# Kernel optimization log

Measured on AMD Instinct MI355X. Metric: run time of the kernel, lower is better.

The kernel has to match this reference:

```python
import jax, jax.numpy as jnp
import numpy as np

N = 10000      # nodes
E = 160000     # edges
F_IN = 128     # input_feature
G = 64         # graphs in batch
NC = 10        # num_classes
H1, H2, H3 = 1000, 700, 200


def _xavier(k, fi, fo):
    lim = float(np.sqrt(6.0 / (fi + fo)))
    return jax.random.uniform(k, (fi, fo), jnp.float32, -lim, lim)


def setup_inputs() -> dict:
    key = jax.random.key(0)
    ks = jax.random.split(key, 8)
    x = jax.random.normal(ks[0], (N, F_IN), jnp.float32)
    edge_index = jax.random.randint(ks[1], (2, E), 0, N)
    batch = jnp.sort(jax.random.randint(ks[2], (N,), 0, G))
    return {
        "x": x,
        "edge_index": edge_index,
        "batch": batch,
        "W1": _xavier(ks[3], F_IN, H1), "b1": jnp.zeros((H1,), jnp.float32),
        "W2": _xavier(ks[4], H1, H2),   "b2": jnp.zeros((H2,), jnp.float32),
        "W3": _xavier(ks[5], H2, H3),   "b3": jnp.zeros((H3,), jnp.float32),
        "Wl": _xavier(ks[6], H3, NC),   "bl": jnp.zeros((NC,), jnp.float32),
    }


def _gcn_conv(x, W, b, src, dst, dinv):
    # GCNConv: h = xW; out_i = sum_{j->i} d_j^-1/2 d_i^-1/2 h_j + d_i^-1 h_i + b
    h = x @ W
    coef = dinv[src] * dinv[dst]                      # [E]
    agg = jax.ops.segment_sum(h[src] * coef[:, None], dst, num_segments=N)
    agg = agg + h * (dinv * dinv)[:, None]            # self-loop term
    return agg + b


def reference(x, edge_index, batch, W1, b1, W2, b2, W3, b3, Wl, bl):
    src, dst = edge_index[0], edge_index[1]
    # degree with self-loops (edge weight 1), computed on target nodes
    deg = jax.ops.segment_sum(jnp.ones((E,), x.dtype), dst, num_segments=N) + 1.0
    dinv = jax.lax.rsqrt(deg)

    h = jax.nn.relu(_gcn_conv(x, W1, b1, src, dst, dinv))
    h = jax.nn.relu(_gcn_conv(h, W2, b2, src, dst, dinv))
    h = jax.nn.relu(_gcn_conv(h, W3, b3, src, dst, dinv))

    # global_mean_pool over graph ids
    s = jax.ops.segment_sum(h, batch, num_segments=G)
    cnt = jax.ops.segment_sum(jnp.ones((N,), h.dtype), batch, num_segments=G)
    pooled = s / jnp.maximum(cnt, 1.0)[:, None]

    # dropout is identity in eval mode
    return pooled @ Wl + bl
```

## Files before the change

### kernel.cpp

```cpp
#include <hip/hip_runtime.h>
#include <hip/hip_bf16.h>
#include <stdint.h>


#define SLOT 64

__device__ __forceinline__ uint16_t f2b(float f) {
    union { float f; uint32_t u; } v; v.f = f;
    return (uint16_t)((v.u + 0x7fffu + ((v.u >> 16) & 1u)) >> 16);
}
__device__ __forceinline__ float blo(uint32_t u) { union { uint32_t u; float f; } v; v.u = u << 16; return v.f; }
__device__ __forceinline__ float bhi(uint32_t u) { union { uint32_t u; float f; } v; v.u = u & 0xffff0000u; return v.f; }

__global__ void k_scatter(const int* __restrict__ src, const int* __restrict__ dst,
                          int* __restrict__ cursor, int* __restrict__ slots, int E) {
    int e = blockIdx.x * blockDim.x + threadIdx.x;
    if (e < E) {
        int s = src[e], d = dst[e];
        int pos = atomicAdd(&cursor[d], 1);
        if (pos < SLOT) slots[d * SLOT + pos] = s;
    }
}
__global__ void k_dinv(const int* __restrict__ deg, float* __restrict__ dinv, int N) {
    int i = blockIdx.x * blockDim.x + threadIdx.x;
    if (i < N) dinv[i] = rsqrtf((float)deg[i] + 1.0f);
}

__global__ void k_prep(const float* __restrict__ W1, const float* __restrict__ W2,
                       const float* __restrict__ W3,
                       uint16_t* __restrict__ T1, uint16_t* __restrict__ T2,
                       uint16_t* __restrict__ T3,
                       const float* __restrict__ b1, const float* __restrict__ b2,
                       const float* __restrict__ b3,
                       float* __restrict__ p1, float* __restrict__ p2,
                       float* __restrict__ p3,
                       const float* __restrict__ x, uint16_t* __restrict__ xb,
                       int F, int H1, int H2, int H3,
                       int Fp, int H1p, int H2p, int H3p, int n8) {
    __shared__ float tile[32][33];
    int z = blockIdx.z;
    if (z < 3) {
        const float* W; uint16_t* T; int K, Nn, Kp, Np;
        if (z == 0)      { W = W1; T = T1; K = F;  Nn = H1; Kp = Fp;  Np = H1p; }
        else if (z == 1) { W = W2; T = T2; K = H1; Nn = H2; Kp = H1p; Np = H2p; }
        else             { W = W3; T = T3; K = H2; Nn = H3; Kp = H2p; Np = H3p; }
        if ((int)blockIdx.x * 32 >= Kp || (int)blockIdx.y * 32 >= Np) return;
        int k0 = blockIdx.x * 32, n0 = blockIdx.y * 32;
        int tx = threadIdx.x, ty = threadIdx.y;
        for (int i = ty; i < 32; i += 8) {
            int k = k0 + i, n = n0 + tx;
            tile[i][tx] = (k < K && n < Nn) ? W[(size_t)k * Nn + n] : 0.f;
        }
        __syncthreads();
        for (int i = ty; i < 32; i += 8) {
            int n = n0 + i, k = k0 + tx;
            T[(size_t)n * Kp + k] = f2b(tile[tx][i]);
        }
    } else {
        int id = (blockIdx.y * gridDim.x + blockIdx.x) * 256 + threadIdx.y * 32 + threadIdx.x;
        if (z == 3) {
            if (id < H1p) p1[id] = (id < H1) ? b1[id] : 0.f;
            else if (id < H1p + H2p) { int k = id - H1p; p2[k] = (k < H2) ? b2[k] : 0.f; }
            else if (id < H1p + H2p + H3p) { int k = id - H1p - H2p; p3[k] = (k < H3) ? b3[k] : 0.f; }
        } else {
            if (id < n8) {
                const float4* x4 = (const float4*)x;
                float4 a = x4[2 * id], b = x4[2 * id + 1];
                uint4 o;
                o.x = (uint32_t)f2b(a.x) | ((uint32_t)f2b(a.y) << 16);
                o.y = (uint32_t)f2b(a.z) | ((uint32_t)f2b(a.w) << 16);
                o.z = (uint32_t)f2b(b.x) | ((uint32_t)f2b(b.y) << 16);
                o.w = (uint32_t)f2b(b.z) | ((uint32_t)f2b(b.w) << 16);
                ((uint4*)xb)[id] = o;
            }
        }
    }
}

__global__ __launch_bounds__(256) void k_agg_panel(
    const uint16_t* __restrict__ in, void* __restrict__ out,
    const int* __restrict__ deg_, const int* __restrict__ slots,
    const float* __restrict__ dinv, const float* __restrict__ bias,
    int N, int Hc, int pc, int P, int relu, int out_f32) {
    int slot  = blockIdx.x & 7;
    int panel = slot % P;
    int seg   = slot / P;
    int nseg  = 8 / P;
    int segLen = (N + nseg - 1) / nseg;
    int idx = (blockIdx.x >> 3) * 256 + threadIdx.x;
    int rel = idx / pc;
    if (rel >= segLen) return;
    int node = seg * segLen + rel;
    if (node >= N) return;
    int j = panel * pc + (idx - rel * pc);
    int deg = deg_[node];
    if (deg > SLOT) deg = SLOT;
    int base = node * SLOT;
    float dv = dinv[node];
    float self = dv * dv;
    const uint4* in4 = (const uint4*)in;
    uint4 v = in4[(size_t)node * Hc + j];
    float a[8];
    a[0] = self * blo(v.x); a[1] = self * bhi(v.x);
    a[2] = self * blo(v.y); a[3] = self * bhi(v.y);
    a[4] = self * blo(v.z); a[5] = self * bhi(v.z);
    a[6] = self * blo(v.w); a[7] = self * bhi(v.w);
    int e = 0;
    for (; e + 2 <= deg; e += 2) {
        int s0 = slots[base + e], s1 = slots[base + e + 1];
        uint4 h0 = in4[(size_t)s0 * Hc + j];
        uint4 h1 = in4[(size_t)s1 * Hc + j];
        float c0 = dinv[s0] * dv, c1 = dinv[s1] * dv;
        a[0] += c0 * blo(h0.x); a[1] += c0 * bhi(h0.x);
        a[2] += c0 * blo(h0.y); a[3] += c0 * bhi(h0.y);
        a[4] += c0 * blo(h0.z); a[5] += c0 * bhi(h0.z);
        a[6] += c0 * blo(h0.w); a[7] += c0 * bhi(h0.w);
        a[0] += c1 * blo(h1.x); a[1] += c1 * bhi(h1.x);
        a[2] += c1 * blo(h1.y); a[3] += c1 * bhi(h1.y);
        a[4] += c1 * blo(h1.z); a[5] += c1 * bhi(h1.z);
        a[6] += c1 * blo(h1.w); a[7] += c1 * bhi(h1.w);
    }
    if (e < deg) {
        int s0 = slots[base + e];
        uint4 h = in4[(size_t)s0 * Hc + j];
        float c = dinv[s0] * dv;
        a[0] += c * blo(h.x); a[1] += c * bhi(h.x);
        a[2] += c * blo(h.y); a[3] += c * bhi(h.y);
        a[4] += c * blo(h.z); a[5] += c * bhi(h.z);
        a[6] += c * blo(h.w); a[7] += c * bhi(h.w);
    }
    if (bias) {
        const float4* b4 = (const float4*)bias;
        float4 b0 = b4[2 * j], b1 = b4[2 * j + 1];
        a[0] += b0.x; a[1] += b0.y; a[2] += b0.z; a[3] += b0.w;
        a[4] += b1.x; a[5] += b1.y; a[6] += b1.z; a[7] += b1.w;
    }
    if (relu) {
#pragma unroll
        for (int t = 0; t < 8; ++t) a[t] = fmaxf(a[t], 0.f);
    }
    if (out_f32) {
        float4* o4 = (float4*)out;
        float4 o0; o0.x = a[0]; o0.y = a[1]; o0.z = a[2]; o0.w = a[3];
        float4 o1; o1.x = a[4]; o1.y = a[5]; o1.z = a[6]; o1.w = a[7];
        o4[(size_t)node * (Hc * 2) + 2 * j]     = o0;
        o4[(size_t)node * (Hc * 2) + 2 * j + 1] = o1;
    } else {
        uint4 o;
        o.x = (uint32_t)f2b(a[0]) | ((uint32_t)f2b(a[1]) << 16);
        o.y = (uint32_t)f2b(a[2]) | ((uint32_t)f2b(a[3]) << 16);
        o.z = (uint32_t)f2b(a[4]) | ((uint32_t)f2b(a[5]) << 16);
        o.w = (uint32_t)f2b(a[6]) | ((uint32_t)f2b(a[7]) << 16);
        ((uint4*)out)[(size_t)node * Hc + j] = o;
    }
}

__global__ __launch_bounds__(256) void k_pool_fast(
    const uint16_t* __restrict__ h, const int* __restrict__ batch,
    float* __restrict__ pooled_sum, int N, int H, int Hp) {
    int j    = threadIdx.x & 63;
    int slot = threadIdx.x >> 6;
    int Hc   = H >> 2;
    if (j >= Hc) return;
    int HcP  = Hp >> 2;
    const uint2* h2 = (const uint2*)h;
    int base = (blockIdx.x * 4 + slot) * 16;
    float a0 = 0.f, a1 = 0.f, a2 = 0.f, a3 = 0.f;
    int gcur = -1;
#pragma unroll 4
    for (int t = 0; t < 16; ++t) {
        int node = base + t;
        if (node < N) {
            int g = batch[node];
            if (g != gcur) {
                if (gcur >= 0) {
                    float* ps = &pooled_sum[(size_t)gcur * H + j * 4];
                    atomicAdd(&ps[0], a0); atomicAdd(&ps[1], a1);
                    atomicAdd(&ps[2], a2); atomicAdd(&ps[3], a3);
                }
                gcur = g; a0 = a1 = a2 = a3 = 0.f;
            }
            uint2 v = h2[(size_t)node * HcP + j];
            a0 += blo(v.x); a1 += bhi(v.x);
            a2 += blo(v.y); a3 += bhi(v.y);
        }
    }
    if (gcur >= 0) {
        float* ps = &pooled_sum[(size_t)gcur * H + j * 4];
        atomicAdd(&ps[0], a0); atomicAdd(&ps[1], a1);
        atomicAdd(&ps[2], a2); atomicAdd(&ps[3], a3);
    }
}

typedef __attribute__((ext_vector_type(8))) short short8;
typedef __attribute__((ext_vector_type(4))) float floatx4;

#define LDSP(p) ((__attribute__((address_space(3))) void*)(uintptr_t)(p))
#define GLBP(p) ((const __attribute__((address_space(1))) void*)(uintptr_t)(p))

__global__ __launch_bounds__(256) void k_gemm_bf16(
    const uint16_t* __restrict__ A, const uint16_t* __restrict__ Bt,
    const float* __restrict__ bias, void* __restrict__ Cout,
    int M, int Kp, int Np, int relu, int out_bf16) {
    __shared__ uint16_t As[128 * 64];
    __shared__ uint16_t Bs[128 * 64];
    int tid = threadIdx.x;
    int wave = tid >> 6, lane = tid & 63;
    int quad = lane >> 4, m16 = lane & 15;
    int wr = wave >> 1, wc = wave & 1;
    int row0 = blockIdx.y * 128, col0 = blockIdx.x * 128;

    int rA = tid >> 3;
    int cA = (tid & 7) ^ (rA & 7);
    const uint16_t* gA = A  + (size_t)(row0 + rA) * Kp + cA * 8;
    const uint16_t* gB = Bt + (size_t)(col0 + rA) * Kp + cA * 8;
    uint16_t* lA = As + tid * 8;
    uint16_t* lB = Bs + tid * 8;
    size_t rowStep32 = (size_t)32 * Kp;

    floatx4 acc[4][4];
#pragma unroll
    for (int i = 0; i < 4; ++i)
#pragma unroll
        for (int j = 0; j < 4; ++j) acc[i][j] = (floatx4){0.f, 0.f, 0.f, 0.f};

    const short* Ash = (const short*)As;
    const short* Bsh = (const short*)Bs;
    int swA = m16 & 7;

    for (int k0 = 0; k0 < Kp; k0 += 64) {
#pragma unroll
        for (int p = 0; p < 4; ++p) {
            __builtin_amdgcn_global_load_lds(GLBP(gA + p * rowStep32), LDSP(lA + p * 2048), 16, 0, 0);
            __builtin_amdgcn_global_load_lds(GLBP(gB + p * rowStep32), LDSP(lB + p * 2048), 16, 0, 0);
        }
        gA += 64; gB += 64;
        __syncthreads();
#pragma unroll
        for (int h = 0; h < 2; ++h) {
            short8 af[4], bf[4];
            int c = h * 4 + quad;
            int pos = (c ^ swA) * 8;
#pragma unroll
            for (int i = 0; i < 4; ++i)
                af[i] = *(const short8*)&Ash[(wr * 64 + i * 16 + m16) * 64 + pos];
#pragma unroll
            for (int j = 0; j < 4; ++j)
                bf[j] = *(const short8*)&Bsh[(wc * 64 + j * 16 + m16) * 64 + pos];
#pragma unroll
            for (int i = 0; i < 4; ++i)
#pragma unroll
                for (int j = 0; j < 4; ++j)
                    acc[i][j] = __builtin_amdgcn_mfma_f32_16x16x32_bf16(af[i], bf[j], acc[i][j], 0, 0, 0);
        }
        __syncthreads();
    }

    float bv[4];
#pragma unroll
    for (int j = 0; j < 4; ++j) {
        int n = col0 + wc * 64 + j * 16 + m16;
        bv[j] = bias ? bias[n] : 0.f;
    }
#pragma unroll
    for (int i = 0; i < 4; ++i) {
        int mBase = row0 + wr * 64 + i * 16 + quad * 4;
#pragma unroll
        for (int r = 0; r < 4; ++r) {
            int m = mBase + r;
            if (m < M) {
#pragma unroll
                for (int j = 0; j < 4; ++j) {
                    int n = col0 + wc * 64 + j * 16 + m16;
                    float v = acc[i][j][r] + bv[j];
                    if (relu) v = fmaxf(v, 0.f);
                    if (out_bf16) ((uint16_t*)Cout)[(size_t)m * Np + n] = f2b(v);
                    else          ((float*)Cout)[(size_t)m * Np + n]    = v;
                }
            }
        }
    }
}

__global__ void k_classifier(const float* __restrict__ pooled_sum,
                             const int* __restrict__ batch,
                             const float* __restrict__ Wl, const float* __restrict__ bl,
                             float* __restrict__ out, int N, int H, int NC) {
    int g = blockIdx.x, c = threadIdx.x;
    int lo = 0, hi = N;
    while (lo < hi) { int mid = (lo + hi) >> 1; if (batch[mid] < g) lo = mid + 1; else hi = mid; }
    int start = lo;
    lo = start; hi = N;
    while (lo < hi) { int mid = (lo + hi) >> 1; if (batch[mid] < g + 1) lo = mid + 1; else hi = mid; }
    int end = lo;
    float scale = 1.0f / fmaxf((float)(end - start), 1.0f);
    if (c < NC) {
        float acc = 0.f;
        for (int k = 0; k < H; ++k) acc += pooled_sum[(size_t)g * H + k] * Wl[(size_t)k * NC + c];
        out[(size_t)g * NC + c] = acc * scale + bl[c];
    }
}

static inline size_t align256(size_t x) { return (x + 255) & ~(size_t)255; }
static inline int pad128(int x) { return (x + 127) & ~127; }

extern "C" void kernel_launch(void* const* d_in, const int* in_sizes, int n_in,
                              void* d_out, int out_size, void* d_ws, size_t ws_size,
                              hipStream_t stream) {
    const float* x   = (const float*)d_in[0];
    const int*   ei  = (const int*)d_in[1];
    const int*   bat = (const int*)d_in[2];
    const float* W1  = (const float*)d_in[3];
    const float* b1  = (const float*)d_in[4];
    const float* W2  = (const float*)d_in[5];
    const float* b2  = (const float*)d_in[6];
    const float* W3  = (const float*)d_in[7];
    const float* b3  = (const float*)d_in[8];
    const float* Wl  = (const float*)d_in[9];
    const float* bl  = (const float*)d_in[10];

    const int N  = in_sizes[2];
    const int E  = in_sizes[1] / 2;
    const int F  = in_sizes[0] / N;
    const int H1 = in_sizes[4];
    const int H2 = in_sizes[6];
    const int H3 = in_sizes[8];
    const int NC = in_sizes[10];
    const int G  = out_size / NC;
    const int* src = ei;
    const int* dst = ei + E;

    const int Mp  = pad128(N);
    const int Fp  = F;
    const int H1p = pad128(H1);
    const int H2p = pad128(H2);
    const int H3p = pad128(H3);

    char* p = (char*)d_ws;
    size_t off = 0;
    auto carve = [&](size_t bytes) { void* q = p + off; off += align256(bytes); return q; };
    uint16_t* xb     = (uint16_t*)carve((size_t)Mp * Fp * 2);
    uint16_t* bufA   = (uint16_t*)carve((size_t)Mp * 2048);
    uint16_t* bufB   = (uint16_t*)carve((size_t)Mp * 2048);
    uint16_t* W1t    = (uint16_t*)carve((size_t)H1p * Fp * 2);
    uint16_t* W2t    = (uint16_t*)carve((size_t)H2p * H1p * 2);
    uint16_t* W3t    = (uint16_t*)carve((size_t)H3p * H2p * 2);
    float* b1p       = (float*)carve((size_t)H1p * 4);
    float* b2p       = (float*)carve((size_t)H2p * 4);
    float* b3p       = (float*)carve((size_t)H3p * 4);
    float* dinv      = (float*)carve((size_t)N * 4);
    int*   cursor    = (int*)carve((size_t)N * 4);
    float* pooled    = (float*)carve((size_t)G * H3 * 4);
    int*   slots     = (int*)carve((size_t)N * SLOT * 4);
    (void)ws_size;

    const int nbN = (N + 255) / 256;
    const int nbE = (E + 255) / 256;

    size_t zlen = (size_t)((char*)pooled - (char*)cursor) + (size_t)G * H3 * 4;
    hipMemsetAsync(cursor, 0, zlen, stream);

    k_scatter<<<nbE, 256, 0, stream>>>(src, dst, cursor, slots, E);
    k_dinv<<<nbN, 256, 0, stream>>>(cursor, dinv, N);

    k_prep<<<dim3(32, 32, 5), dim3(32, 8), 0, stream>>>(
        W1, W2, W3, W1t, W2t, W3t, b1, b2, b3, b1p, b2p, b3p, x, xb,
        F, H1, H2, H3, Fp, H1p, H2p, H3p, N * F / 8);

    auto agg_grid = [&](int P, int pc) {
        int nseg = 8 / P;
        int segLen = (N + nseg - 1) / nseg;
        return 8 * ((segLen * pc + 255) / 256);
    };

    k_agg_panel<<<agg_grid(1, 16), 256, 0, stream>>>(
        xb, bufA, cursor, slots, dinv, nullptr, N, 16, 16, 1, 0, 0);
    k_gemm_bf16<<<dim3(H1p / 128, Mp / 128), 256, 0, stream>>>(
        bufA, W1t, b1p, bufB, N, Fp, H1p, 1, 1);

    k_gemm_bf16<<<dim3(H2p / 128, Mp / 128), 256, 0, stream>>>(
        bufB, W2t, nullptr, bufA, N, H1p, H2p, 0, 1);
    k_agg_panel<<<agg_grid(8, 12), 256, 0, stream>>>(
        bufA, bufB, cursor, slots, dinv, b2p, N, 96, 12, 8, 1, 0);

    k_gemm_bf16<<<dim3(H3p / 128, Mp / 128), 256, 0, stream>>>(
        bufB, W3t, nullptr, bufA, N, H2p, H3p, 0, 1);
    k_agg_panel<<<agg_grid(4, 8), 256, 0, stream>>>(
        bufA, bufB, cursor, slots, dinv, b3p, N, 32, 8, 4, 1, 0);

    k_pool_fast<<<(N + 63) / 64, 256, 0, stream>>>(
        (const uint16_t*)bufB, bat, pooled, N, H3, H3p);
    k_classifier<<<G, 64, 0, stream>>>(pooled, bat, Wl, bl, (float*)d_out, N, H3, NC);
}
```

Measured before the change: 257.3 us.

## Split neighbor aggregation across half-waves and shrink GEMM N-tile to 64

The aggregation kernel now gives each (node, chunk) item two half-wave lanes, each summing half of the neighbor list, and combines them with a cross-lane shuffle before bias, ReLU and bf16 store. This doubles memory-level parallelism on the irregular gathers at the cost of twice as many threads and an extra shuffle. The unused f32 output path is removed. Separately, the bf16 MFMA GEMM tile is narrowed from 128x128 to 128x64, doubling the block count for the small-N layers (H3 in particular) to improve CU occupancy. The price is lower per-block reuse of the A tile.

```diff
diff --git a/kernel.cpp b/kernel.cpp
--- a/kernel.cpp
+++ b/kernel.cpp
@@ -78,35 +78,41 @@
 }
 
 __global__ __launch_bounds__(256) void k_agg_panel(
-    const uint16_t* __restrict__ in, void* __restrict__ out,
+    const uint16_t* __restrict__ in, uint16_t* __restrict__ out,
     const int* __restrict__ deg_, const int* __restrict__ slots,
     const float* __restrict__ dinv, const float* __restrict__ bias,
-    int N, int Hc, int pc, int P, int relu, int out_f32) {
-    int slot  = blockIdx.x & 7;
-    int panel = slot % P;
-    int seg   = slot / P;
+    int N, int Hc, int pc, int P, int relu) {
+    int slotg = blockIdx.x & 7;
+    int panel = slotg % P;
+    int seg   = slotg / P;
     int nseg  = 8 / P;
     int segLen = (N + nseg - 1) / nseg;
-    int idx = (blockIdx.x >> 3) * 256 + threadIdx.x;
-    int rel = idx / pc;
+    int wave = threadIdx.x >> 6, lane = threadIdx.x & 63;
+    int half = lane >> 5, sub = lane & 31;
+    int item = (blockIdx.x >> 3) * 128 + wave * 32 + sub;
+    int rel = item / pc;
     if (rel >= segLen) return;
     int node = seg * segLen + rel;
     if (node >= N) return;
-    int j = panel * pc + (idx - rel * pc);
+    int j = panel * pc + (item - rel * pc);
     int deg = deg_[node];
     if (deg > SLOT) deg = SLOT;
+    int dh = (deg + 1) >> 1;
+    int e  = half ? dh : 0;
+    int eE = half ? deg : dh;
     int base = node * SLOT;
     float dv = dinv[node];
-    float self = dv * dv;
     const uint4* in4 = (const uint4*)in;
-    uint4 v = in4[(size_t)node * Hc + j];
-    float a[8];
-    a[0] = self * blo(v.x); a[1] = self * bhi(v.x);
-    a[2] = self * blo(v.y); a[3] = self * bhi(v.y);
-    a[4] = self * blo(v.z); a[5] = self * bhi(v.z);
-    a[6] = self * blo(v.w); a[7] = self * bhi(v.w);
-    int e = 0;
-    for (; e + 2 <= deg; e += 2) {
+    float a[8] = {0.f, 0.f, 0.f, 0.f, 0.f, 0.f, 0.f, 0.f};
+    if (half == 0) {
+        float self = dv * dv;
+        uint4 v = in4[(size_t)node * Hc + j];
+        a[0] = self * blo(v.x); a[1] = self * bhi(v.x);
+        a[2] = self * blo(v.y); a[3] = self * bhi(v.y);
+        a[4] = self * blo(v.z); a[5] = self * bhi(v.z);
+        a[6] = self * blo(v.w); a[7] = self * bhi(v.w);
+    }
+    for (; e + 2 <= eE; e += 2) {
         int s0 = slots[base + e], s1 = slots[base + e + 1];
         uint4 h0 = in4[(size_t)s0 * Hc + j];
         uint4 h1 = in4[(size_t)s1 * Hc + j];
@@ -120,7 +126,7 @@
         a[4] += c1 * blo(h1.z); a[5] += c1 * bhi(h1.z);
         a[6] += c1 * blo(h1.w); a[7] += c1 * bhi(h1.w);
     }
-    if (e < deg) {
+    if (e < eE) {
         int s0 = slots[base + e];
         uint4 h = in4[(size_t)s0 * Hc + j];
         float c = dinv[s0] * dv;
@@ -129,23 +135,19 @@
         a[4] += c * blo(h.z); a[5] += c * bhi(h.z);
         a[6] += c * blo(h.w); a[7] += c * bhi(h.w);
     }
-    if (bias) {
-        const float4* b4 = (const float4*)bias;
-        float4 b0 = b4[2 * j], b1 = b4[2 * j + 1];
-        a[0] += b0.x; a[1] += b0.y; a[2] += b0.z; a[3] += b0.w;
-        a[4] += b1.x; a[5] += b1.y; a[6] += b1.z; a[7] += b1.w;
-    }
-    if (relu) {
-#pragma unroll
-        for (int t = 0; t < 8; ++t) a[t] = fmaxf(a[t], 0.f);
-    }
-    if (out_f32) {
-        float4* o4 = (float4*)out;
-        float4 o0; o0.x = a[0]; o0.y = a[1]; o0.z = a[2]; o0.w = a[3];
-        float4 o1; o1.x = a[4]; o1.y = a[5]; o1.z = a[6]; o1.w = a[7];
-        o4[(size_t)node * (Hc * 2) + 2 * j]     = o0;
-        o4[(size_t)node * (Hc * 2) + 2 * j + 1] = o1;
-    } else {
+#pragma unroll
+    for (int t = 0; t < 8; ++t) a[t] += __shfl_xor(a[t], 32, 64);
+    if (half == 0) {
+        if (bias) {
+            const float4* b4 = (const float4*)bias;
+            float4 b0 = b4[2 * j], b1 = b4[2 * j + 1];
+            a[0] += b0.x; a[1] += b0.y; a[2] += b0.z; a[3] += b0.w;
+            a[4] += b1.x; a[5] += b1.y; a[6] += b1.z; a[7] += b1.w;
+        }
+        if (relu) {
+#pragma unroll
+            for (int t = 0; t < 8; ++t) a[t] = fmaxf(a[t], 0.f);
+        }
         uint4 o;
         o.x = (uint32_t)f2b(a[0]) | ((uint32_t)f2b(a[1]) << 16);
         o.y = (uint32_t)f2b(a[2]) | ((uint32_t)f2b(a[3]) << 16);
@@ -203,12 +205,12 @@
     const float* __restrict__ bias, void* __restrict__ Cout,
     int M, int Kp, int Np, int relu, int out_bf16) {
     __shared__ uint16_t As[128 * 64];
-    __shared__ uint16_t Bs[128 * 64];
+    __shared__ uint16_t Bs[64 * 64];
     int tid = threadIdx.x;
     int wave = tid >> 6, lane = tid & 63;
     int quad = lane >> 4, m16 = lane & 15;
     int wr = wave >> 1, wc = wave & 1;
-    int row0 = blockIdx.y * 128, col0 = blockIdx.x * 128;
+    int row0 = blockIdx.y * 128, col0 = blockIdx.x * 64;
 
     int rA = tid >> 3;
     int cA = (tid & 7) ^ (rA & 7);
@@ -218,11 +220,11 @@
     uint16_t* lB = Bs + tid * 8;
     size_t rowStep32 = (size_t)32 * Kp;
 
-    floatx4 acc[4][4];
+    floatx4 acc[4][2];
 #pragma unroll
     for (int i = 0; i < 4; ++i)
 #pragma unroll
-        for (int j = 0; j < 4; ++j) acc[i][j] = (floatx4){0.f, 0.f, 0.f, 0.f};
+        for (int j = 0; j < 2; ++j) acc[i][j] = (floatx4){0.f, 0.f, 0.f, 0.f};
 
     const short* Ash = (const short*)As;
     const short* Bsh = (const short*)Bs;
@@ -230,36 +232,37 @@
 
     for (int k0 = 0; k0 < Kp; k0 += 64) {
 #pragma unroll
-        for (int p = 0; p < 4; ++p) {
+        for (int p = 0; p < 4; ++p)
             __builtin_amdgcn_global_load_lds(GLBP(gA + p * rowStep32), LDSP(lA + p * 2048), 16, 0, 0);
+#pragma unroll
+        for (int p = 0; p < 2; ++p)
             __builtin_amdgcn_global_load_lds(GLBP(gB + p * rowStep32), LDSP(lB + p * 2048), 16, 0, 0);
-        }
         gA += 64; gB += 64;
         __syncthreads();
 #pragma unroll
         for (int h = 0; h < 2; ++h) {
-            short8 af[4], bf[4];
+            short8 af[4], bf[2];
             int c = h * 4 + quad;
             int pos = (c ^ swA) * 8;
 #pragma unroll
             for (int i = 0; i < 4; ++i)
                 af[i] = *(const short8*)&Ash[(wr * 64 + i * 16 + m16) * 64 + pos];
 #pragma unroll
-            for (int j = 0; j < 4; ++j)
-                bf[j] = *(const short8*)&Bsh[(wc * 64 + j * 16 + m16) * 64 + pos];
+            for (int j = 0; j < 2; ++j)
+                bf[j] = *(const short8*)&Bsh[(wc * 32 + j * 16 + m16) * 64 + pos];
 #pragma unroll
             for (int i = 0; i < 4; ++i)
 #pragma unroll
-                for (int j = 0; j < 4; ++j)
+                for (int j = 0; j < 2; ++j)
                     acc[i][j] = __builtin_amdgcn_mfma_f32_16x16x32_bf16(af[i], bf[j], acc[i][j], 0, 0, 0);
         }
         __syncthreads();
     }
 
-    float bv[4];
-#pragma unroll
-    for (int j = 0; j < 4; ++j) {
-        int n = col0 + wc * 64 + j * 16 + m16;
+    float bv[2];
+#pragma unroll
+    for (int j = 0; j < 2; ++j) {
+        int n = col0 + wc * 32 + j * 16 + m16;
         bv[j] = bias ? bias[n] : 0.f;
     }
 #pragma unroll
@@ -270,8 +273,8 @@
             int m = mBase + r;
             if (m < M) {
 #pragma unroll
-                for (int j = 0; j < 4; ++j) {
-                    int n = col0 + wc * 64 + j * 16 + m16;
+                for (int j = 0; j < 2; ++j) {
+                    int n = col0 + wc * 32 + j * 16 + m16;
                     float v = acc[i][j][r] + bv[j];
                     if (relu) v = fmaxf(v, 0.f);
                     if (out_bf16) ((uint16_t*)Cout)[(size_t)m * Np + n] = f2b(v);
@@ -370,23 +373,23 @@
     auto agg_grid = [&](int P, int pc) {
         int nseg = 8 / P;
         int segLen = (N + nseg - 1) / nseg;
-        return 8 * ((segLen * pc + 255) / 256);
+        return 8 * ((segLen * pc + 127) / 128);
     };
 
     k_agg_panel<<<agg_grid(1, 16), 256, 0, stream>>>(
-        xb, bufA, cursor, slots, dinv, nullptr, N, 16, 16, 1, 0, 0);
-    k_gemm_bf16<<<dim3(H1p / 128, Mp / 128), 256, 0, stream>>>(
+        xb, bufA, cursor, slots, dinv, nullptr, N, 16, 16, 1, 0);
+    k_gemm_bf16<<<dim3(H1p / 64, Mp / 128), 256, 0, stream>>>(
         bufA, W1t, b1p, bufB, N, Fp, H1p, 1, 1);
 
-    k_gemm_bf16<<<dim3(H2p / 128, Mp / 128), 256, 0, stream>>>(
+    k_gemm_bf16<<<dim3(H2p / 64, Mp / 128), 256, 0, stream>>>(
         bufB, W2t, nullptr, bufA, N, H1p, H2p, 0, 1);
     k_agg_panel<<<agg_grid(8, 12), 256, 0, stream>>>(
-        bufA, bufB, cursor, slots, dinv, b2p, N, 96, 12, 8, 1, 0);
-
-    k_gemm_bf16<<<dim3(H3p / 128, Mp / 128), 256, 0, stream>>>(
+        bufA, bufB, cursor, slots, dinv, b2p, N, 96, 12, 8, 1);
+
+    k_gemm_bf16<<<dim3(H3p / 64, Mp / 128), 256, 0, stream>>>(
         bufB, W3t, nullptr, bufA, N, H2p, H3p, 0, 1);
     k_agg_panel<<<agg_grid(4, 8), 256, 0, stream>>>(
-        bufA, bufB, cursor, slots, dinv, b3p, N, 32, 8, 4, 1, 0);
+        bufA, bufB, cursor, slots, dinv, b3p, N, 32, 8, 4, 1);
 
     k_pool_fast<<<(N + 63) / 64, 256, 0, stream>>>(
         (const uint16_t*)bufB, bat, pooled, N, H3, H3p);
```

Measured after the change: 255.3 us. About the same (-0.8%).
